# Kernel optimization log

Hardware: AMD Instinct MI355X
Metric: run time of the kernel (lower is better)

The kernel has to match this reference:

```python
import jax, jax.numpy as jnp
import numpy as np

DEPTH, DIM, DIN, DM, NST, RNK, CSTEM, NCLS = 4, 64, 128, 256, 16, 8, 32, 16
EPS = 1e-5


def silu(x):
    return x * jax.nn.sigmoid(x)


def layernorm(x, g, b):
    m = x.mean(-1, keepdims=True)
    v = x.var(-1, keepdims=True)
    return (x - m) / jnp.sqrt(v + EPS) * g + b


def bn3d(x, g, b, m, v):  # eval-mode BatchNorm3d, x [B,C,T,H,W]
    s = g / jnp.sqrt(v + EPS)
    return x * s[None, :, None, None, None] + (b - m * s)[None, :, None, None, None]


def dwconv3d_same(x, w, b):  # x [B,C,T,H,W], w [C,1,3,3,3]
    y = jax.lax.conv_general_dilated(x, w, (1, 1, 1), 'SAME',
                                     feature_group_count=x.shape[1],
                                     dimension_numbers=('NCDHW', 'OIDHW', 'NCDHW'))
    return y + b[None, :, None, None, None]


def mamba(u, in_w, conv_w, conv_b, xproj_w, dtproj_w, dtproj_b, Alog, Dp, out_w):
    # u: [b, L, DIN]; mamba_ssm Mamba(d_model=DIN, d_state=16, expand=2, d_conv=4)
    b, L, _ = u.shape
    xz = u @ in_w.T                                  # [b,L,2*DM]
    x, z = jnp.split(xz, 2, axis=-1)                 # [b,L,DM] each
    # causal depthwise conv1d, kernel 4, left-pad 3
    xc = jnp.moveaxis(x, 1, 2)                       # [b,DM,L]
    xc = jnp.pad(xc, ((0, 0), (0, 0), (3, 0)))
    xc = jax.lax.conv_general_dilated(xc, conv_w, (1,), 'VALID',
                                      feature_group_count=conv_w.shape[0],
                                      dimension_numbers=('NCH', 'OIH', 'NCH'))
    xc = xc + conv_b[None, :, None]
    x = silu(jnp.moveaxis(xc, 2, 1))                 # [b,L,DM]
    dbc = x @ xproj_w.T                              # [b,L,RNK+2*NST]
    dt, Bc, Cc = jnp.split(dbc, [RNK, RNK + NST], axis=-1)
    dt = jax.nn.softplus(dt @ dtproj_w.T + dtproj_b)  # [b,L,DM]
    A = -jnp.exp(Alog)                               # [DM,NST]

    def step(h, inp):
        dt_l, u_l, B_l, C_l = inp                    # [b,DM],[b,DM],[b,NST],[b,NST]
        dA = jnp.exp(dt_l[..., None] * A)            # [b,DM,NST]
        h = dA * h + (dt_l * u_l)[..., None] * B_l[:, None, :]
        y = jnp.einsum('bdn,bn->bd', h, C_l)
        return h, y

    xs = (jnp.moveaxis(dt, 1, 0), jnp.moveaxis(x, 1, 0),
          jnp.moveaxis(Bc, 1, 0), jnp.moveaxis(Cc, 1, 0))
    h0 = jnp.zeros((b, DM, NST), x.dtype)
    _, ys = jax.lax.scan(step, h0, xs)               # ys [L,b,DM]
    y = jnp.moveaxis(ys, 0, 1) + x * Dp              # D skip
    y = y * silu(z)
    return y @ out_w.T                               # [b,L,DIN]


def setup_inputs() -> dict:
    key = jax.random.key(0)
    ks = iter(jax.random.split(key, 64))

    def rn(shape, s=0.02):
        return jax.random.normal(next(ks), shape, jnp.float32) * s

    D = DEPTH
    inp = {
        'x': jax.random.normal(next(ks), (32, 1, 32, 13, 13), jnp.float32),
        # R(2+1)D stem
        'sconv_w': rn((CSTEM, 1, 1, 3, 3), 0.1),
        'bn1_g': jnp.ones((CSTEM,)), 'bn1_b': jnp.zeros((CSTEM,)),
        'bn1_m': rn((CSTEM,), 0.1),
        'bn1_v': jax.random.uniform(next(ks), (CSTEM,), jnp.float32, 0.5, 1.5),
        'tconv_w': rn((CSTEM, 1, 3, 1, 1), 0.2),
        'bn2_g': jnp.ones((CSTEM,)), 'bn2_b': jnp.zeros((CSTEM,)),
        'bn2_m': rn((CSTEM,), 0.1),
        'bn2_v': jax.random.uniform(next(ks), (CSTEM,), jnp.float32, 0.5, 1.5),
        'last_w': rn((2 * CSTEM, CSTEM, 1, 1, 1), 0.1),
        # per-block params, stacked over depth
        'ln1_g': jnp.ones((D, DIM)), 'ln1_b': jnp.zeros((D, DIM)),
        'in_proj_w': rn((D, 2 * DIN, DIM)),
        'conv3d_w': rn((D, DIN, 1, 3, 3, 3), 0.1), 'conv3d_b': rn((D, DIN), 0.1),
        'm_in_w': rn((D, 2 * DM, DIN)),
        'm_conv_w': rn((D, DM, 1, 4), 0.2), 'm_conv_b': rn((D, DM), 0.1),
        'm_xproj_w': rn((D, RNK + 2 * NST, DM)),
        'm_dtproj_w': rn((D, DM, RNK), 0.1), 'm_dtproj_b': rn((D, DM), 0.1),
        'm_Alog': jnp.log(jax.random.uniform(next(ks), (D, DM, NST), jnp.float32, 1.0, 16.0)),
        'm_D': jnp.ones((D, DM)),
        'm_out_w': rn((D, DIN, DM)),
        'out_proj_w': rn((D, DIM, DIN)),
        'ln2_g': jnp.ones((D, DIM)), 'ln2_b': jnp.zeros((D, DIM)),
        'fc1_w': rn((D, 4 * DIM, DIM)), 'fc1_b': rn((D, 4 * DIM), 0.1),
        'fc2_w': rn((D, DIM, 4 * DIM)), 'fc2_b': rn((D, DIM), 0.1),
        'head_w': rn((NCLS, DIM)), 'head_b': jnp.zeros((NCLS,)),
    }
    return inp


def reference(x, sconv_w, bn1_g, bn1_b, bn1_m, bn1_v, tconv_w, bn2_g, bn2_b, bn2_m,
              bn2_v, last_w, ln1_g, ln1_b, in_proj_w, conv3d_w, conv3d_b, m_in_w,
              m_conv_w, m_conv_b, m_xproj_w, m_dtproj_w, m_dtproj_b, m_Alog, m_D,
              m_out_w, out_proj_w, ln2_g, ln2_b, fc1_w, fc1_b, fc2_w, fc2_b,
              head_w, head_b):
    dn = ('NCDHW', 'OIDHW', 'NCDHW')
    # R(2+1)D stem: spatial conv -> BN -> ReLU -> temporal dwconv -> BN -> ReLU -> 1x1x1
    h = jax.lax.conv_general_dilated(x, sconv_w, (1, 1, 1), 'VALID', dimension_numbers=dn)
    h = jax.nn.relu(bn3d(h, bn1_g, bn1_b, bn1_m, bn1_v))
    h = jax.lax.conv_general_dilated(h, tconv_w, (1, 1, 1), 'VALID',
                                     feature_group_count=CSTEM, dimension_numbers=dn)
    h = jax.nn.relu(bn3d(h, bn2_g, bn2_b, bn2_m, bn2_v))
    h = jax.lax.conv_general_dilated(h, last_w, (1, 1, 1), 'VALID', dimension_numbers=dn)
    xb = jnp.transpose(h, (0, 2, 3, 4, 1))  # [B, T', H', W', DIM]

    for i in range(DEPTH):
        # --- SSM branch ---
        hx = layernorm(xb, ln1_g[i], ln1_b[i])
        xz = hx @ in_proj_w[i].T                       # [B,T,H,W,2*DIN]
        xs_, z = jnp.split(xz, 2, axis=-1)
        z = silu(z)
        xc = jnp.moveaxis(xs_, 4, 1)                   # [B,DIN,T,H,W]
        xc = silu(dwconv3d_same(xc, conv3d_w[i], conv3d_b[i]))
        b, c, t, hh, ww = xc.shape
        seq = jnp.moveaxis(xc.reshape(b, c, t * hh * ww), 1, 2)  # [B,L,DIN]
        seq2 = jnp.concatenate([seq, seq[:, ::-1]], axis=0)      # [2B,L,DIN]
        y2 = mamba(seq2, m_in_w[i], m_conv_w[i], m_conv_b[i], m_xproj_w[i],
                   m_dtproj_w[i], m_dtproj_b[i], m_Alog[i], m_D[i], m_out_w[i])
        y = y2[:b] + y2[b:, ::-1]
        y = y.reshape(b, t, hh, ww, c) * z
        xb = xb + y @ out_proj_w[i].T
        # --- MLP branch ---
        h2 = layernorm(xb, ln2_g[i], ln2_b[i])
        h2 = jax.nn.gelu(h2 @ fc1_w[i].T + fc1_b[i], approximate=False)
        xb = xb + h2 @ fc2_w[i].T + fc2_b[i]

    feature = xb.mean(axis=(1, 2, 3))                  # [B, DIM]
    logits = feature @ head_w.T + head_b               # [B, NCLS]
    return (logits, feature)
```

## Files before the change

kernel.cpp:

```cpp
#include <hip/hip_runtime.h>
#include <hip/hip_bf16.h>
#include <hip/hip_fp16.h>

#define LL    3630
#define EPSV  1e-5f
#define NCH   57
#define CLEN  64

typedef short bf16x8 __attribute__((ext_vector_type(8)));
typedef float f32x4  __attribute__((ext_vector_type(4)));
typedef float f32x2  __attribute__((ext_vector_type(2)));
typedef float f32x16 __attribute__((ext_vector_type(16)));

__device__ __forceinline__ float bf2f(__hip_bfloat16 x){ return __bfloat162float(x); }
__device__ __forceinline__ __hip_bfloat16 f2bf(float x){ return __float2bfloat16(x); }
__device__ __forceinline__ float siluf(float x){ return x / (1.f + __expf(-x)); }
__device__ __forceinline__ float s2f(short s){ __hip_bfloat16 t = __builtin_bit_cast(__hip_bfloat16, s); return __bfloat162float(t); }
__device__ __forceinline__ short f2s(float x){ __hip_bfloat16 t = __float2bfloat16(x); return __builtin_bit_cast(short, t); }

__global__ __launch_bounds__(256) void convert_weights(
    const float* __restrict__ s0, const float* __restrict__ s1,
    const float* __restrict__ s2, const float* __restrict__ s3,
    const float* __restrict__ s4, const float* __restrict__ s5,
    const float* __restrict__ s6,
    __hip_bfloat16* __restrict__ dst)
{
  int gid = blockIdx.x*256 + threadIdx.x;
  float v;
  if      (gid <  65536) v = s0[gid];
  else if (gid < 327680) v = s1[gid-65536];
  else if (gid < 458752) v = s2[gid-327680];
  else if (gid < 491520) v = s3[gid-458752];
  else if (gid < 557056) v = s4[gid-491520];
  else if (gid < 622592) v = s5[gid-557056];
  else if (gid < 671744){
    int rel = gid - 622592;
    int layer = rel / 12288;
    int rr  = (rel % 12288) / 256;
    int ccol= rel & 255;
    v = (rr < 40) ? s6[layer*10240 + rr*256 + ccol] : 0.f;
  }
  else return;
  dst[gid] = f2bf(v);
}

__global__ __launch_bounds__(256) void stem1_kernel(
    const float* __restrict__ x, const float* __restrict__ w,
    const float* __restrict__ g, const float* __restrict__ bb,
    const float* __restrict__ mm, const float* __restrict__ vv,
    float* __restrict__ out, int nb, int b0)
{
  int idx = blockIdx.x*256 + threadIdx.x;
  if (idx >= nb*123904) return;
  int j = idx % 11;
  int i = (idx/11) % 11;
  int t = (idx/121) % 32;
  int c = (idx/(121*32)) % 32;
  int b = idx/(121*32*32);
  const float* xp = x + ((b0+b)*32 + t)*169;
  const float* wp = w + c*9;
  float acc = 0.f;
  #pragma unroll
  for (int di=0; di<3; ++di)
    #pragma unroll
    for (int dj=0; dj<3; ++dj)
      acc += xp[(i+di)*13 + (j+dj)] * wp[di*3+dj];
  float s = g[c]*rsqrtf(vv[c]+EPSV);
  acc = acc*s + (bb[c]-mm[c]*s);
  out[idx] = fmaxf(acc, 0.f);
}

__global__ __launch_bounds__(256) void stem2_kernel(
    const float* __restrict__ h1, const float* __restrict__ w,
    const float* __restrict__ g, const float* __restrict__ bb,
    const float* __restrict__ mm, const float* __restrict__ vv,
    float* __restrict__ out, int nb)
{
  int idx = blockIdx.x*256 + threadIdx.x;
  if (idx >= nb*116160) return;
  int ij = idx % 121;
  int t  = (idx/121) % 30;
  int c  = (idx/(121*30)) % 32;
  int b  = idx/(121*30*32);
  const float* hp = h1 + ((b*32+c)*32)*121 + ij;
  const float* wp = w + c*3;
  float acc = 0.f;
  #pragma unroll
  for (int k=0;k<3;++k) acc += hp[(t+k)*121] * wp[k];
  float s = g[c]*rsqrtf(vv[c]+EPSV);
  acc = acc*s + (bb[c]-mm[c]*s);
  out[idx] = fmaxf(acc, 0.f);
}

__global__ __launch_bounds__(256) void stem3_kernel(
    const float* __restrict__ h2, const float* __restrict__ w,
    __hip_bfloat16* __restrict__ xb, int tokens)
{
  int gid = blockIdx.x*256 + threadIdx.x;
  int cc = gid & 63;
  int tok = gid >> 6;
  if (tok >= tokens) return;
  int ij = tok % 121;
  int t  = (tok/121) % 30;
  int b  = tok/LL;
  const float* hp = h2 + ((long)b*32)*30*121 + t*121 + ij;
  const float* wp = w + cc*32;
  float acc = 0.f;
  #pragma unroll
  for (int ci=0; ci<32; ++ci) acc += hp[ci*3630] * wp[ci];
  xb[(long)tok*64+cc] = f2bf(acc);
}

__global__ __launch_bounds__(256) void ln_kernel(
    const __hip_bfloat16* __restrict__ xb, const float* __restrict__ g,
    const float* __restrict__ b2, __hip_bfloat16* __restrict__ out, int tokens)
{
  int wid = threadIdx.x >> 6, lane = threadIdx.x & 63;
  long tok = (long)blockIdx.x*4 + wid;
  if (tok >= tokens) return;
  float v = bf2f(xb[tok*64 + lane]);
  float s = v, q = v*v;
  #pragma unroll
  for (int m=1; m<64; m<<=1){ s += __shfl_xor(s,m); q += __shfl_xor(q,m); }
  float mean = s*(1.f/64.f);
  float var  = q*(1.f/64.f) - mean*mean;
  float o = (v-mean)*rsqrtf(var+EPSV)*g[lane] + b2[lane];
  out[tok*64+lane] = f2bf(o);
}

template<int EPI>
__global__ __launch_bounds__(256) void gemm_bf16(
    const __hip_bfloat16* __restrict__ A, const __hip_bfloat16* __restrict__ W,
    int K, int N, int NH, int tokens,
    __hip_bfloat16* __restrict__ out1, __hip_bfloat16* __restrict__ out2,
    const float* __restrict__ bias, const __hip_bfloat16* __restrict__ gate,
    __hip_bfloat16* __restrict__ resid,
    const float* __restrict__ lng, const float* __restrict__ lnb)
{
  int w   = threadIdx.x >> 6;
  int lane= threadIdx.x & 63;
  int r16 = lane & 15;
  int kg  = lane >> 4;
  long m0 = (long)blockIdx.x*128 + w*32;
  int  n0 = blockIdx.y*64;
  long ra0 = m0 + r16;      if (ra0 > tokens-1) ra0 = tokens-1;
  long ra1 = m0 + 16 + r16; if (ra1 > tokens-1) ra1 = tokens-1;
  f32x4 acc[2][4] = { { {0,0,0,0},{0,0,0,0},{0,0,0,0},{0,0,0,0} },
                      { {0,0,0,0},{0,0,0,0},{0,0,0,0},{0,0,0,0} } };
  for (int k0 = 0; k0 < K; k0 += 32){
    bf16x8 a0 = *reinterpret_cast<const bf16x8*>(A + ra0*K + k0 + kg*8);
    bf16x8 a1 = *reinterpret_cast<const bf16x8*>(A + ra1*K + k0 + kg*8);
    #pragma unroll
    for (int f=0; f<4; ++f){
      bf16x8 b = *reinterpret_cast<const bf16x8*>(W + (long)(n0 + f*16 + r16)*K + k0 + kg*8);
      acc[0][f] = __builtin_amdgcn_mfma_f32_16x16x32_bf16(a0, b, acc[0][f], 0, 0, 0);
      acc[1][f] = __builtin_amdgcn_mfma_f32_16x16x32_bf16(a1, b, acc[1][f], 0, 0, 0);
    }
  }
  if (EPI == 5){
    float gv[4], bv[4], biasv[4];
    #pragma unroll
    for (int f=0; f<4; ++f){
      gv[f] = lng[f*16+r16]; bv[f] = lnb[f*16+r16];
      biasv[f] = bias ? bias[f*16+r16] : 0.f;
    }
    #pragma unroll
    for (int g2=0; g2<2; ++g2){
      #pragma unroll
      for (int r=0; r<4; ++r){
        long row = m0 + g2*16 + kg*4 + r;
        bool ok = row < tokens;
        long rowc = ok ? row : (tokens-1);
        float v[4]; float s = 0.f, q = 0.f;
        #pragma unroll
        for (int f=0; f<4; ++f){
          float t = acc[g2][f][r] + biasv[f] + bf2f(resid[rowc*64 + f*16+r16]);
          v[f] = t; s += t; q += t*t;
        }
        #pragma unroll
        for (int m=1; m<16; m<<=1){ s += __shfl_xor(s,m); q += __shfl_xor(q,m); }
        float mean = s*(1.f/64.f);
        float var  = q*(1.f/64.f) - mean*mean;
        float rstd = rsqrtf(var+EPSV);
        if (ok){
          #pragma unroll
          for (int f=0; f<4; ++f){
            resid[row*64 + f*16+r16] = f2bf(v[f]);
            out1 [row*64 + f*16+r16] = f2bf((v[f]-mean)*rstd*gv[f] + bv[f]);
          }
        }
      }
    }
    return;
  }
  #pragma unroll
  for (int g2=0; g2<2; ++g2){
    #pragma unroll
    for (int f=0; f<4; ++f){
      int col = n0 + f*16 + r16;
      #pragma unroll
      for (int r=0; r<4; ++r){
        long row = m0 + g2*16 + kg*4 + r;
        if (row >= tokens) continue;
        float v = acc[g2][f][r];
        if (EPI == 0){
          if (col < NH) out1[row*NH + col] = f2bf(v);
          else          out2[row*NH + col - NH] = f2bf(siluf(v));
        } else if (EPI == 2){
          v += bias[col];
          v = 0.5f*v*(1.f + erff(v*0.70710678118f));
          out1[row*N + col] = f2bf(v);
        } else if (EPI == 3){
          if (bias) v += bias[col];
          resid[row*N + col] = f2bf(v + bf2f(resid[row*N + col]));
        } else {
          out1[row*N + col] = f2bf(v * bf2f(gate[row*N + col]));
        }
      }
    }
  }
}

__global__ __launch_bounds__(256) void dwconv3d_kernel(
    const __hip_bfloat16* __restrict__ xs, const float* __restrict__ w,
    const float* __restrict__ bias, __hip_bfloat16* __restrict__ seq, int tokens)
{
  long gid = (long)blockIdx.x*256 + threadIdx.x;
  int c = gid & 127;
  long tok = gid >> 7;
  if (tok >= tokens) return;
  int j  = tok % 11;
  int i2 = (tok/11) % 11;
  int t  = (tok/121) % 30;
  long b = tok/LL;
  const float* wc = w + c*27;
  float acc = bias[c];
  #pragma unroll
  for (int dt=0; dt<3; ++dt){
    int tt = t+dt-1; if (tt<0 || tt>=30) continue;
    #pragma unroll
    for (int di=0; di<3; ++di){
      int ii = i2+di-1; if (ii<0 || ii>=11) continue;
      #pragma unroll
      for (int dj=0; dj<3; ++dj){
        int jj = j+dj-1; if (jj<0 || jj>=11) continue;
        long t2 = (b*30+tt)*121 + ii*11 + jj;
        acc += wc[dt*9+di*3+dj] * bf2f(xs[t2*128 + c]);
      }
    }
  }
  seq[tok*128 + c] = f2bf(siluf(acc));
}

__global__ __launch_bounds__(256) void mamba_pre_scan(
    const __hip_bfloat16* __restrict__ xm,
    const float* __restrict__ cw, const float* __restrict__ cbv,
    const __hip_bfloat16* __restrict__ xpw_bf,
    const float* __restrict__ dtw, const float* __restrict__ dtbv,
    const float* __restrict__ Alog,
    __hip_bfloat16* __restrict__ ub,
    float* __restrict__ pre,
    float* __restrict__ hfin, float* __restrict__ sdt,
    int nb)
{
  __shared__ __hip_bfloat16 xcs[64][264];
  __shared__ float pres[64][44];
  int s  = blockIdx.x / NCH;
  int ch = blockIdx.x % NCH;
  int p0 = ch*CLEN;
  int b  = s % nb;
  bool fwd = s < nb;
  int d = threadIdx.x;
  const long basex = (long)b*LL*256 + d;
  const long sLL = (long)s*LL;
  {
    float w0=cw[d*4], w1=cw[d*4+1], w2=cw[d*4+2], w3=cw[d*4+3], cb=cbv[d];
    float p1=0.f, p2=0.f, p3=0.f;
    if (p0-1 >= 0) p1 = bf2f(xm[basex + (long)(fwd ? p0-1 : LL-p0  )*256]);
    if (p0-2 >= 0) p2 = bf2f(xm[basex + (long)(fwd ? p0-2 : LL+1-p0)*256]);
    if (p0-3 >= 0) p3 = bf2f(xm[basex + (long)(fwd ? p0-3 : LL+2-p0)*256]);
    for (int t=0; t<64; ++t){
      int p = p0 + t;
      float xl = 0.f;
      if (p < LL) xl = bf2f(xm[basex + (long)(fwd ? p : LL-1-p)*256]);
      float xc = w3*xl + w2*p1 + w1*p2 + w0*p3 + cb;
      p3=p2; p2=p1; p1=xl;
      __hip_bfloat16 uv = f2bf(siluf(xc));
      xcs[t][d] = uv;
      if (p < LL) ub[(sLL + p)*256 + d] = uv;
    }
  }
  __syncthreads();
  {
    int w = threadIdx.x >> 6, lane = threadIdx.x & 63;
    int r16 = lane & 15, kg = lane >> 4;
    int t0 = w*16;
    f32x4 acc[3] = { {0,0,0,0},{0,0,0,0},{0,0,0,0} };
    for (int k0=0; k0<256; k0+=32){
      bf16x8 a = *reinterpret_cast<const bf16x8*>(&xcs[t0+r16][k0+kg*8]);
      #pragma unroll
      for (int f=0; f<3; ++f){
        bf16x8 bb = *reinterpret_cast<const bf16x8*>(xpw_bf + (f*16+r16)*256 + k0 + kg*8);
        acc[f] = __builtin_amdgcn_mfma_f32_16x16x32_bf16(a, bb, acc[f], 0, 0, 0);
      }
    }
    #pragma unroll
    for (int f=0; f<3; ++f){
      int col = f*16 + r16;
      #pragma unroll
      for (int r=0; r<4; ++r){
        int tl = t0 + kg*4 + r;
        int p = p0 + tl;
        if (col < 40){
          pres[tl][col] = acc[f][r];
          if (p < LL) pre[(sLL + p)*40 + col] = acc[f][r];
        }
      }
    }
  }
  __syncthreads();
  {
    int lim = LL - p0; if (lim > CLEN) lim = CLEN;
    f32x2 a2[8], h[8];
    #pragma unroll
    for (int k=0;k<8;++k){
      a2[k] = (f32x2){ -__expf(Alog[d*16+2*k])*1.44269504f,
                       -__expf(Alog[d*16+2*k+1])*1.44269504f };
      h[k] = (f32x2){0.f, 0.f};
    }
    float dw[8];
    #pragma unroll
    for (int r=0;r<8;++r) dw[r] = dtw[d*8+r];
    float dtb_d = dtbv[d];
    float sacc = 0.f;
    for (int t=0; t<lim; ++t){
      float u = bf2f(xcs[t][d]);
      float4 r0 = *reinterpret_cast<const float4*>(&pres[t][0]);
      float4 r1 = *reinterpret_cast<const float4*>(&pres[t][4]);
      float xacc = dtb_d;
      xacc = fmaf(r0.x,dw[0],fmaf(r0.y,dw[1],fmaf(r0.z,dw[2],fmaf(r0.w,dw[3],xacc))));
      xacc = fmaf(r1.x,dw[4],fmaf(r1.y,dw[5],fmaf(r1.z,dw[6],fmaf(r1.w,dw[7],xacc))));
      float dt = (xacc > 20.f) ? xacc : __logf(1.f + __expf(xacc));
      sacc += dt;
      float4 B0 = *reinterpret_cast<const float4*>(&pres[t][8]);
      float4 B1 = *reinterpret_cast<const float4*>(&pres[t][12]);
      float4 B2 = *reinterpret_cast<const float4*>(&pres[t][16]);
      float4 B3 = *reinterpret_cast<const float4*>(&pres[t][20]);
      float Bv[16] = {B0.x,B0.y,B0.z,B0.w,B1.x,B1.y,B1.z,B1.w,
                      B2.x,B2.y,B2.z,B2.w,B3.x,B3.y,B3.z,B3.w};
      f32x2 dt2  = (f32x2){dt, dt};
      float dtu = dt*u;
      f32x2 dtu2 = (f32x2){dtu, dtu};
      #pragma unroll
      for (int k=0;k<8;++k){
        f32x2 tt = dt2*a2[k];
        f32x2 e = (f32x2){ exp2f(tt.x), exp2f(tt.y) };
        f32x2 bk = (f32x2){ Bv[2*k], Bv[2*k+1] };
        h[k] = __builtin_elementwise_fma(e, h[k], dtu2*bk);
      }
    }
    long hbase = ((long)blockIdx.x*256 + d)*16;
    #pragma unroll
    for (int k=0;k<8;++k){ hfin[hbase+2*k] = h[k].x; hfin[hbase+2*k+1] = h[k].y; }
    sdt[(long)blockIdx.x*256 + d] = sacc;
  }
}

__global__ __launch_bounds__(256) void scan_comb(
    const float* __restrict__ Alog,
    float* __restrict__ hfin, const float* __restrict__ sdt)
{
  int s = blockIdx.x >> 4, dg = blockIdx.x & 15;
  int d = dg*16 + (threadIdx.x >> 4), n = threadIdx.x & 15;
  float a2 = -__expf(Alog[d*16+n]) * 1.44269504f;
  float h = 0.f;
  for (int ch=0; ch<NCH; ++ch){
    long sc = (long)s*NCH + ch;
    long idx = (sc*256 + d)*16 + n;
    float hf = hfin[idx];
    float sd = sdt[sc*256 + d];
    hfin[idx] = h;
    h = exp2f(a2*sd)*h + hf;
  }
}

__global__ __launch_bounds__(256) void scan_p2(
    __hip_bfloat16* __restrict__ ub,
    const float* __restrict__ pre,
    const float* __restrict__ dtw, const float* __restrict__ dtbv,
    const float* __restrict__ Alog, const float* __restrict__ Dv,
    const float* __restrict__ hinit)
{
  int d = threadIdx.x;
  int sc = blockIdx.x;
  int ch = sc % NCH, s = sc / NCH;
  int l0 = ch*CLEN;
  int lim = LL - l0; if (lim > CLEN) lim = CLEN;
  f32x2 a2[8], h[8];
  long hbase = ((long)sc*256 + d)*16;
  #pragma unroll
  for (int k=0;k<8;++k){
    a2[k] = (f32x2){ -__expf(Alog[d*16+2*k])*1.44269504f,
                     -__expf(Alog[d*16+2*k+1])*1.44269504f };
    h[k] = (f32x2){ hinit[hbase+2*k], hinit[hbase+2*k+1] };
  }
  float dw[8];
  #pragma unroll
  for (int r=0;r<8;++r) dw[r] = dtw[d*8+r];
  float dtb_d = dtbv[d];
  float dpv = Dv[d];
  long tok0 = (long)s*LL + l0;
  long ui = tok0*256 + d;
  long pi = tok0*40;
  for (int l=0; l<lim; ++l){
    float u = bf2f(ub[ui]);
    float4 r0 = *reinterpret_cast<const float4*>(pre+pi);
    float4 r1 = *reinterpret_cast<const float4*>(pre+pi+4);
    float xacc = dtb_d;
    xacc = fmaf(r0.x,dw[0],fmaf(r0.y,dw[1],fmaf(r0.z,dw[2],fmaf(r0.w,dw[3],xacc))));
    xacc = fmaf(r1.x,dw[4],fmaf(r1.y,dw[5],fmaf(r1.z,dw[6],fmaf(r1.w,dw[7],xacc))));
    float dt = (xacc > 20.f) ? xacc : __logf(1.f + __expf(xacc));
    f32x16 B = *reinterpret_cast<const f32x16*>(pre+pi+8);
    f32x16 C = *reinterpret_cast<const f32x16*>(pre+pi+24);
    f32x2 dt2  = (f32x2){dt, dt};
    float dtu = dt*u;
    f32x2 dtu2 = (f32x2){dtu, dtu};
    f32x2 y2 = (f32x2){0.f, 0.f};
    #pragma unroll
    for (int k=0;k<8;++k){
      f32x2 t = dt2*a2[k];
      f32x2 e = (f32x2){ exp2f(t.x), exp2f(t.y) };
      f32x2 bk = (f32x2){ B[2*k], B[2*k+1] };
      f32x2 ck = (f32x2){ C[2*k], C[2*k+1] };
      h[k] = __builtin_elementwise_fma(e, h[k], dtu2*bk);
      y2 = __builtin_elementwise_fma(h[k], ck, y2);
    }
    float y = y2.x + y2.y;
    ub[ui] = f2bf(y + u*dpv);
    ui += 256; pi += 40;
  }
}

__global__ __launch_bounds__(256) void combine_kernel(
    const __hip_bfloat16* __restrict__ yb, const __hip_bfloat16* __restrict__ zm,
    __hip_bfloat16* __restrict__ ycomb, int tokens, int nb)
{
  long gid = (long)blockIdx.x*256 + threadIdx.x;
  long tok = gid >> 5;
  if (tok >= tokens) return;
  int c8 = (gid & 31) * 8;
  long l = tok % LL, b = tok / LL;
  bf16x8 vf = *reinterpret_cast<const bf16x8*>(yb + ( b*LL + l)*256 + c8);
  bf16x8 vb = *reinterpret_cast<const bf16x8*>(yb + ((nb+b)*LL + (LL-1-l))*256 + c8);
  bf16x8 zz = *reinterpret_cast<const bf16x8*>(zm + tok*256 + c8);
  bf16x8 out;
  #pragma unroll
  for (int k=0;k<8;++k){
    float r = (s2f(vf[k]) + s2f(vb[k])) * s2f(zz[k]);
    out[k] = f2s(r);
  }
  *reinterpret_cast<bf16x8*>(ycomb + tok*256 + c8) = out;
}

__global__ __launch_bounds__(256) void head1_kernel(
    const __hip_bfloat16* __restrict__ xb, float* __restrict__ hp)
{
  __shared__ float partial[4][64];
  int b = blockIdx.x / 30, ch = blockIdx.x % 30;
  int d = threadIdx.x & 63, part = threadIdx.x >> 6;
  float acc = 0.f;
  int lend = (ch+1)*121;
  for (int l = ch*121 + part; l < lend; l += 4)
    acc += bf2f(xb[((long)b*LL + l)*64 + d]);
  partial[part][d] = acc;
  __syncthreads();
  if (part == 0)
    hp[(b*30 + ch)*64 + d] = partial[0][d]+partial[1][d]+partial[2][d]+partial[3][d];
}

__global__ __launch_bounds__(64) void head2_kernel(
    const float* __restrict__ hp, const float* __restrict__ hw,
    const float* __restrict__ hb, float* __restrict__ out, int b0)
{
  __shared__ float feat[64];
  int b = blockIdx.x;
  int d = threadIdx.x;
  float acc = 0.f;
  #pragma unroll
  for (int ch=0; ch<30; ++ch) acc += hp[(b*30+ch)*64 + d];
  float f = acc * (1.f/3630.f);
  feat[d] = f;
  out[512 + (b0+b)*64 + d] = f;
  __syncthreads();
  if (d < 16){
    float a2 = hb[d];
    #pragma unroll
    for (int k=0; k<64; ++k) a2 += feat[k]*hw[d*64+k];
    out[(b0+b)*16 + d] = a2;
  }
}

extern "C" void kernel_launch(void* const* d_in, const int* in_sizes, int n_in,
                              void* d_out, int out_size, void* d_ws, size_t ws_size,
                              hipStream_t stream)
{
  const float* x        = (const float*)d_in[0];
  const float* sconv_w  = (const float*)d_in[1];
  const float* bn1_g    = (const float*)d_in[2];
  const float* bn1_b    = (const float*)d_in[3];
  const float* bn1_m    = (const float*)d_in[4];
  const float* bn1_v    = (const float*)d_in[5];
  const float* tconv_w  = (const float*)d_in[6];
  const float* bn2_g    = (const float*)d_in[7];
  const float* bn2_b    = (const float*)d_in[8];
  const float* bn2_m    = (const float*)d_in[9];
  const float* bn2_v    = (const float*)d_in[10];
  const float* last_w   = (const float*)d_in[11];
  const float* ln1_g    = (const float*)d_in[12];
  const float* ln1_b    = (const float*)d_in[13];
  const float* in_proj_w= (const float*)d_in[14];
  const float* conv3d_w = (const float*)d_in[15];
  const float* conv3d_b = (const float*)d_in[16];
  const float* m_in_w   = (const float*)d_in[17];
  const float* m_conv_w = (const float*)d_in[18];
  const float* m_conv_b = (const float*)d_in[19];
  const float* m_xproj_w= (const float*)d_in[20];
  const float* m_dtproj_w=(const float*)d_in[21];
  const float* m_dtproj_b=(const float*)d_in[22];
  const float* m_Alog   = (const float*)d_in[23];
  const float* m_D      = (const float*)d_in[24];
  const float* m_out_w  = (const float*)d_in[25];
  const float* out_proj_w=(const float*)d_in[26];
  const float* ln2_g    = (const float*)d_in[27];
  const float* ln2_b    = (const float*)d_in[28];
  const float* fc1_w    = (const float*)d_in[29];
  const float* fc1_b    = (const float*)d_in[30];
  const float* fc2_w    = (const float*)d_in[31];
  const float* fc2_b    = (const float*)d_in[32];
  const float* head_w   = (const float*)d_in[33];
  const float* head_b   = (const float*)d_in[34];

  const size_t WB = 1345536;
  int nb = 1;
  for (int cand = 32; cand >= 1; cand >>= 1){
    size_t TPc = (((size_t)cand*LL + 63)/64)*64;
    size_t S2c = (size_t)2*cand*LL;
    size_t need = WB + TPc*2048 + S2c*672;
    if (need <= ws_size){ nb = cand; break; }
  }
  const size_t TP  = (((size_t)nb*LL + 63)/64)*64;
  const int S2  = 2*nb;
  const size_t S2T = (size_t)S2*LL;
  const int tokens = nb*LL;

  char* ws = (char*)d_ws;
  __hip_bfloat16* wbf   = (__hip_bfloat16*)(ws);
  size_t o = WB;
  __hip_bfloat16* xb    = (__hip_bfloat16*)(ws + o); o += TP*128;
  __hip_bfloat16* hx    = (__hip_bfloat16*)(ws + o); o += TP*128;
  float*          hp    = (float*)hx;
  float*          hfin  = (float*)hx;
  __hip_bfloat16* xs    = (__hip_bfloat16*)(ws + o); o += TP*256;
  __hip_bfloat16* seq   = (__hip_bfloat16*)(ws + o); o += TP*256;
  __hip_bfloat16* ycomb = xs;
  __hip_bfloat16* zblk  = (__hip_bfloat16*)(ws + o); o += TP*256;
  __hip_bfloat16* xm    = (__hip_bfloat16*)(ws + o);
  __hip_bfloat16* yo    = xm;                        o += TP*512;
  __hip_bfloat16* zm    = (__hip_bfloat16*)(ws + o);
  __hip_bfloat16* h2m   = zm;                        o += TP*512;
  float*          pre   = (float*)(ws + o);          o += S2T*160;
  __hip_bfloat16* ybuf  = (__hip_bfloat16*)(ws + o);
  float*          h1s   = (float*)(ws + o);
  float*          h2s   = (float*)(ws + o + (size_t)nb*495616);
  float*          sdtb  = hfin + (size_t)S2*NCH*4096;

  convert_weights<<<2624, 256, 0, stream>>>(in_proj_w, m_in_w, m_out_w, out_proj_w,
                                            fc1_w, fc2_w, m_xproj_w, wbf);

  const int gM2 = (int)((TP + 127)/128);

  for (int b0 = 0; b0 < 32; b0 += nb){
    stem1_kernel<<<nb*484, 256, 0, stream>>>(x, sconv_w, bn1_g, bn1_b, bn1_m, bn1_v, h1s, nb, b0);
    stem2_kernel<<<(nb*116160+255)/256, 256, 0, stream>>>(h1s, tconv_w, bn2_g, bn2_b, bn2_m, bn2_v, h2s, nb);
    stem3_kernel<<<(tokens*64+255)/256, 256, 0, stream>>>(h2s, last_w, xb, tokens);
    ln_kernel<<<(tokens+3)/4, 256, 0, stream>>>(xb, ln1_g, ln1_b, hx, tokens);

    for (int i = 0; i < 4; ++i){
      gemm_bf16<0><<<dim3(gM2,4), 256, 0, stream>>>(hx, wbf + i*16384, 64, 256, 128, tokens,
                                                    xs, zblk, nullptr, nullptr, nullptr, nullptr, nullptr);
      dwconv3d_kernel<<<(tokens*128+255)/256, 256, 0, stream>>>(xs, conv3d_w + i*3456, conv3d_b + i*128, seq, tokens);
      gemm_bf16<0><<<dim3(gM2,8), 256, 0, stream>>>(seq, wbf + 65536 + i*65536, 128, 512, 256, tokens,
                                                    xm, zm, nullptr, nullptr, nullptr, nullptr, nullptr);
      mamba_pre_scan<<<S2*NCH, 256, 0, stream>>>(xm, m_conv_w + i*1024, m_conv_b + i*256,
                                                 wbf + 622592 + i*12288,
                                                 m_dtproj_w + i*2048, m_dtproj_b + i*256,
                                                 m_Alog + i*4096,
                                                 ybuf, pre, hfin, sdtb, nb);
      scan_comb<<<S2*16, 256, 0, stream>>>(m_Alog + i*4096, hfin, sdtb);
      scan_p2<<<S2*NCH, 256, 0, stream>>>(ybuf, pre, m_dtproj_w + i*2048, m_dtproj_b + i*256,
                                          m_Alog + i*4096, m_D + i*256, hfin);
      combine_kernel<<<(tokens*32+255)/256, 256, 0, stream>>>(ybuf, zm, ycomb, tokens, nb);
      gemm_bf16<4><<<dim3(gM2,2), 256, 0, stream>>>(ycomb, wbf + 327680 + i*32768, 256, 128, 0, tokens,
                                                    yo, nullptr, nullptr, zblk, nullptr, nullptr, nullptr);
      gemm_bf16<5><<<dim3(gM2,1), 256, 0, stream>>>(yo, wbf + 458752 + i*8192, 128, 64, 0, tokens,
                                                    hx, nullptr, nullptr, nullptr, xb,
                                                    ln2_g + i*64, ln2_b + i*64);
      gemm_bf16<2><<<dim3(gM2,4), 256, 0, stream>>>(hx, wbf + 491520 + i*16384, 64, 256, 0, tokens,
                                                    h2m, nullptr, fc1_b + i*256, nullptr, nullptr, nullptr, nullptr);
      int inext = (i < 3) ? i+1 : 3;
      gemm_bf16<5><<<dim3(gM2,1), 256, 0, stream>>>(h2m, wbf + 557056 + i*16384, 256, 64, 0, tokens,
                                                    hx, nullptr, fc2_b + i*64, nullptr, xb,
                                                    ln1_g + inext*64, ln1_b + inext*64);
    }
    head1_kernel<<<nb*30, 256, 0, stream>>>(xb, hp);
    head2_kernel<<<nb, 64, 0, stream>>>(hp, head_w, head_b, (float*)d_out, b0);
  }
}
```

Measured before the change: 6.192 ms.

## Enlarge GEMM row tile, remap blocks across XCDs, drop shared-memory staging in pre-scan

The bf16 MFMA GEMM now has each wave compute 64 rows instead of 32, so every block covers 256 rows. Each loaded B fragment is reused across four A fragments, which cuts weight reloads per FLOP. The 2D grid becomes a 1D grid with an XCD-aware remap, so neighbouring tiles that share A rows land on the same XCD's L2. In mamba_pre_scan, the LDS copy of the x-projection results is removed and the scan loop reads them back from the global pre buffer, relying on cache hits. The larger tile raises register pressure and halves the grid size, and the global re-reads may cost more than the saved LDS.

```diff
diff --git a/kernel.cpp b/kernel.cpp
--- a/kernel.cpp
+++ b/kernel.cpp
@@ -131,7 +131,7 @@
 template<int EPI>
 __global__ __launch_bounds__(256) void gemm_bf16(
     const __hip_bfloat16* __restrict__ A, const __hip_bfloat16* __restrict__ W,
-    int K, int N, int NH, int tokens,
+    int K, int N, int NH, int ny, int tokens,
     __hip_bfloat16* __restrict__ out1, __hip_bfloat16* __restrict__ out2,
     const float* __restrict__ bias, const __hip_bfloat16* __restrict__ gate,
     __hip_bfloat16* __restrict__ resid,
@@ -141,21 +141,39 @@
   int lane= threadIdx.x & 63;
   int r16 = lane & 15;
   int kg  = lane >> 4;
-  long m0 = (long)blockIdx.x*128 + w*32;
-  int  n0 = blockIdx.y*64;
-  long ra0 = m0 + r16;      if (ra0 > tokens-1) ra0 = tokens-1;
-  long ra1 = m0 + 16 + r16; if (ra1 > tokens-1) ra1 = tokens-1;
-  f32x4 acc[2][4] = { { {0,0,0,0},{0,0,0,0},{0,0,0,0},{0,0,0,0} },
-                      { {0,0,0,0},{0,0,0,0},{0,0,0,0},{0,0,0,0} } };
+  int nwg = gridDim.x;
+  int orig = blockIdx.x;
+  int q = nwg >> 3, r8 = nwg & 7;
+  int xcd = orig & 7, off = orig >> 3;
+  int wg = (xcd < r8 ? xcd*(q+1) : r8*(q+1) + (xcd-r8)*q) + off;
+  int by = wg % ny;
+  long bx = wg / ny;
+  long m0 = bx*256 + w*64;
+  int  n0 = by*64;
+  long ra[4];
+  #pragma unroll
+  for (int fr=0; fr<4; ++fr){
+    long t = m0 + fr*16 + r16;
+    ra[fr] = (t > tokens-1) ? (long)(tokens-1) : t;
+  }
+  f32x4 acc[4][4];
+  #pragma unroll
+  for (int fr=0; fr<4; ++fr)
+    #pragma unroll
+    for (int f=0; f<4; ++f) acc[fr][f] = (f32x4){0,0,0,0};
   for (int k0 = 0; k0 < K; k0 += 32){
-    bf16x8 a0 = *reinterpret_cast<const bf16x8*>(A + ra0*K + k0 + kg*8);
-    bf16x8 a1 = *reinterpret_cast<const bf16x8*>(A + ra1*K + k0 + kg*8);
-    #pragma unroll
-    for (int f=0; f<4; ++f){
-      bf16x8 b = *reinterpret_cast<const bf16x8*>(W + (long)(n0 + f*16 + r16)*K + k0 + kg*8);
-      acc[0][f] = __builtin_amdgcn_mfma_f32_16x16x32_bf16(a0, b, acc[0][f], 0, 0, 0);
-      acc[1][f] = __builtin_amdgcn_mfma_f32_16x16x32_bf16(a1, b, acc[1][f], 0, 0, 0);
-    }
+    bf16x8 a[4], b[4];
+    #pragma unroll
+    for (int fr=0; fr<4; ++fr)
+      a[fr] = *reinterpret_cast<const bf16x8*>(A + ra[fr]*K + k0 + kg*8);
+    #pragma unroll
+    for (int f=0; f<4; ++f)
+      b[f] = *reinterpret_cast<const bf16x8*>(W + (long)(n0 + f*16 + r16)*K + k0 + kg*8);
+    #pragma unroll
+    for (int fr=0; fr<4; ++fr)
+      #pragma unroll
+      for (int f=0; f<4; ++f)
+        acc[fr][f] = __builtin_amdgcn_mfma_f32_16x16x32_bf16(a[fr], b[f], acc[fr][f], 0, 0, 0);
   }
   if (EPI == 5){
     float gv[4], bv[4], biasv[4];
@@ -165,22 +183,22 @@
       biasv[f] = bias ? bias[f*16+r16] : 0.f;
     }
     #pragma unroll
-    for (int g2=0; g2<2; ++g2){
+    for (int fr=0; fr<4; ++fr){
       #pragma unroll
       for (int r=0; r<4; ++r){
-        long row = m0 + g2*16 + kg*4 + r;
+        long row = m0 + fr*16 + kg*4 + r;
         bool ok = row < tokens;
         long rowc = ok ? row : (tokens-1);
-        float v[4]; float s = 0.f, q = 0.f;
+        float v[4]; float s = 0.f, qq = 0.f;
         #pragma unroll
         for (int f=0; f<4; ++f){
-          float t = acc[g2][f][r] + biasv[f] + bf2f(resid[rowc*64 + f*16+r16]);
-          v[f] = t; s += t; q += t*t;
+          float t = acc[fr][f][r] + biasv[f] + bf2f(resid[rowc*64 + f*16+r16]);
+          v[f] = t; s += t; qq += t*t;
         }
         #pragma unroll
-        for (int m=1; m<16; m<<=1){ s += __shfl_xor(s,m); q += __shfl_xor(q,m); }
+        for (int m=1; m<16; m<<=1){ s += __shfl_xor(s,m); qq += __shfl_xor(qq,m); }
         float mean = s*(1.f/64.f);
-        float var  = q*(1.f/64.f) - mean*mean;
+        float var  = qq*(1.f/64.f) - mean*mean;
         float rstd = rsqrtf(var+EPSV);
         if (ok){
           #pragma unroll
@@ -194,15 +212,15 @@
     return;
   }
   #pragma unroll
-  for (int g2=0; g2<2; ++g2){
+  for (int fr=0; fr<4; ++fr){
     #pragma unroll
     for (int f=0; f<4; ++f){
       int col = n0 + f*16 + r16;
       #pragma unroll
       for (int r=0; r<4; ++r){
-        long row = m0 + g2*16 + kg*4 + r;
+        long row = m0 + fr*16 + kg*4 + r;
         if (row >= tokens) continue;
-        float v = acc[g2][f][r];
+        float v = acc[fr][f][r];
         if (EPI == 0){
           if (col < NH) out1[row*NH + col] = f2bf(v);
           else          out2[row*NH + col - NH] = f2bf(siluf(v));
@@ -210,9 +228,6 @@
           v += bias[col];
           v = 0.5f*v*(1.f + erff(v*0.70710678118f));
           out1[row*N + col] = f2bf(v);
-        } else if (EPI == 3){
-          if (bias) v += bias[col];
-          resid[row*N + col] = f2bf(v + bf2f(resid[row*N + col]));
         } else {
           out1[row*N + col] = f2bf(v * bf2f(gate[row*N + col]));
         }
@@ -264,7 +279,6 @@
     int nb)
 {
   __shared__ __hip_bfloat16 xcs[64][264];
-  __shared__ float pres[64][44];
   int s  = blockIdx.x / NCH;
   int ch = blockIdx.x % NCH;
   int p0 = ch*CLEN;
@@ -311,10 +325,7 @@
       for (int r=0; r<4; ++r){
         int tl = t0 + kg*4 + r;
         int p = p0 + tl;
-        if (col < 40){
-          pres[tl][col] = acc[f][r];
-          if (p < LL) pre[(sLL + p)*40 + col] = acc[f][r];
-        }
+        if (col < 40 && p < LL) pre[(sLL + p)*40 + col] = acc[f][r];
       }
     }
   }
@@ -333,19 +344,21 @@
     for (int r=0;r<8;++r) dw[r] = dtw[d*8+r];
     float dtb_d = dtbv[d];
     float sacc = 0.f;
+    const float* pb = pre + (sLL + p0)*40;
     for (int t=0; t<lim; ++t){
       float u = bf2f(xcs[t][d]);
-      float4 r0 = *reinterpret_cast<const float4*>(&pres[t][0]);
-      float4 r1 = *reinterpret_cast<const float4*>(&pres[t][4]);
+      const float* pt = pb + (long)t*40;
+      float4 r0 = *reinterpret_cast<const float4*>(pt);
+      float4 r1 = *reinterpret_cast<const float4*>(pt+4);
       float xacc = dtb_d;
       xacc = fmaf(r0.x,dw[0],fmaf(r0.y,dw[1],fmaf(r0.z,dw[2],fmaf(r0.w,dw[3],xacc))));
       xacc = fmaf(r1.x,dw[4],fmaf(r1.y,dw[5],fmaf(r1.z,dw[6],fmaf(r1.w,dw[7],xacc))));
       float dt = (xacc > 20.f) ? xacc : __logf(1.f + __expf(xacc));
       sacc += dt;
-      float4 B0 = *reinterpret_cast<const float4*>(&pres[t][8]);
-      float4 B1 = *reinterpret_cast<const float4*>(&pres[t][12]);
-      float4 B2 = *reinterpret_cast<const float4*>(&pres[t][16]);
-      float4 B3 = *reinterpret_cast<const float4*>(&pres[t][20]);
+      float4 B0 = *reinterpret_cast<const float4*>(pt+8);
+      float4 B1 = *reinterpret_cast<const float4*>(pt+12);
+      float4 B2 = *reinterpret_cast<const float4*>(pt+16);
+      float4 B3 = *reinterpret_cast<const float4*>(pt+20);
       float Bv[16] = {B0.x,B0.y,B0.z,B0.w,B1.x,B1.y,B1.z,B1.w,
                       B2.x,B2.y,B2.z,B2.w,B3.x,B3.y,B3.z,B3.w};
       f32x2 dt2  = (f32x2){dt, dt};
@@ -577,7 +590,7 @@
   convert_weights<<<2624, 256, 0, stream>>>(in_proj_w, m_in_w, m_out_w, out_proj_w,
                                             fc1_w, fc2_w, m_xproj_w, wbf);
 
-  const int gM2 = (int)((TP + 127)/128);
+  const int gMB = (int)((TP + 255)/256);
 
   for (int b0 = 0; b0 < 32; b0 += nb){
     stem1_kernel<<<nb*484, 256, 0, stream>>>(x, sconv_w, bn1_g, bn1_b, bn1_m, bn1_v, h1s, nb, b0);
@@ -586,11 +599,11 @@
     ln_kernel<<<(tokens+3)/4, 256, 0, stream>>>(xb, ln1_g, ln1_b, hx, tokens);
 
     for (int i = 0; i < 4; ++i){
-      gemm_bf16<0><<<dim3(gM2,4), 256, 0, stream>>>(hx, wbf + i*16384, 64, 256, 128, tokens,
-                                                    xs, zblk, nullptr, nullptr, nullptr, nullptr, nullptr);
+      gemm_bf16<0><<<gMB*4, 256, 0, stream>>>(hx, wbf + i*16384, 64, 256, 128, 4, tokens,
+                                              xs, zblk, nullptr, nullptr, nullptr, nullptr, nullptr);
       dwconv3d_kernel<<<(tokens*128+255)/256, 256, 0, stream>>>(xs, conv3d_w + i*3456, conv3d_b + i*128, seq, tokens);
-      gemm_bf16<0><<<dim3(gM2,8), 256, 0, stream>>>(seq, wbf + 65536 + i*65536, 128, 512, 256, tokens,
-                                                    xm, zm, nullptr, nullptr, nullptr, nullptr, nullptr);
+      gemm_bf16<0><<<gMB*8, 256, 0, stream>>>(seq, wbf + 65536 + i*65536, 128, 512, 256, 8, tokens,
+                                              xm, zm, nullptr, nullptr, nullptr, nullptr, nullptr);
       mamba_pre_scan<<<S2*NCH, 256, 0, stream>>>(xm, m_conv_w + i*1024, m_conv_b + i*256,
                                                  wbf + 622592 + i*12288,
                                                  m_dtproj_w + i*2048, m_dtproj_b + i*256,
@@ -600,17 +613,17 @@
       scan_p2<<<S2*NCH, 256, 0, stream>>>(ybuf, pre, m_dtproj_w + i*2048, m_dtproj_b + i*256,
                                           m_Alog + i*4096, m_D + i*256, hfin);
       combine_kernel<<<(tokens*32+255)/256, 256, 0, stream>>>(ybuf, zm, ycomb, tokens, nb);
-      gemm_bf16<4><<<dim3(gM2,2), 256, 0, stream>>>(ycomb, wbf + 327680 + i*32768, 256, 128, 0, tokens,
-                                                    yo, nullptr, nullptr, zblk, nullptr, nullptr, nullptr);
-      gemm_bf16<5><<<dim3(gM2,1), 256, 0, stream>>>(yo, wbf + 458752 + i*8192, 128, 64, 0, tokens,
-                                                    hx, nullptr, nullptr, nullptr, xb,
-                                                    ln2_g + i*64, ln2_b + i*64);
-      gemm_bf16<2><<<dim3(gM2,4), 256, 0, stream>>>(hx, wbf + 491520 + i*16384, 64, 256, 0, tokens,
-                                                    h2m, nullptr, fc1_b + i*256, nullptr, nullptr, nullptr, nullptr);
+      gemm_bf16<4><<<gMB*2, 256, 0, stream>>>(ycomb, wbf + 327680 + i*32768, 256, 128, 0, 2, tokens,
+                                              yo, nullptr, nullptr, zblk, nullptr, nullptr, nullptr);
+      gemm_bf16<5><<<gMB, 256, 0, stream>>>(yo, wbf + 458752 + i*8192, 128, 64, 0, 1, tokens,
+                                            hx, nullptr, nullptr, nullptr, xb,
+                                            ln2_g + i*64, ln2_b + i*64);
+      gemm_bf16<2><<<gMB*4, 256, 0, stream>>>(hx, wbf + 491520 + i*16384, 64, 256, 0, 4, tokens,
+                                              h2m, nullptr, fc1_b + i*256, nullptr, nullptr, nullptr, nullptr);
       int inext = (i < 3) ? i+1 : 3;
-      gemm_bf16<5><<<dim3(gM2,1), 256, 0, stream>>>(h2m, wbf + 557056 + i*16384, 256, 64, 0, tokens,
-                                                    hx, nullptr, fc2_b + i*64, nullptr, xb,
-                                                    ln1_g + inext*64, ln1_b + inext*64);
+      gemm_bf16<5><<<gMB, 256, 0, stream>>>(h2m, wbf + 557056 + i*16384, 256, 64, 0, 1, tokens,
+                                            hx, nullptr, fc2_b + i*64, nullptr, xb,
+                                            ln1_g + inext*64, ln1_b + inext*64);
     }
     head1_kernel<<<nb*30, 256, 0, stream>>>(xb, hp);
     head2_kernel<<<nb, 64, 0, stream>>>(hp, head_w, head_b, (float*)d_out, b0);
```

After: 6.500 ms. 5.0% more time.
